# Performance work log

Hardware: AMD Instinct MI355X
Metric: run time of the kernel (lower is better)

The kernel has to match this reference:

```python
import jax, jax.numpy as jnp
import numpy as np

ALPHA = 0.1  # relu_alpha

def leaky(v, a=ALPHA):
    return jnp.where(v > 0, v, a * v)

def setup_inputs() -> dict:
    key = jax.random.key(0)
    ks = jax.random.split(key, 12)
    N, D, E, H = 50000, 128, 800000, 256
    x = jax.random.normal(ks[0], (N, D), dtype=jnp.float32)
    edge_index = jax.random.randint(ks[1], (2, E), 0, N, dtype=jnp.int64)
    def lin(k, i, o):
        s = 1.0 / np.sqrt(i)
        return jax.random.uniform(k, (i, o), jnp.float32, -s, s)
    return {
        "x": x,
        "edge_index": edge_index,
        "W_gcn": lin(ks[2], D, 512), "b_gcn": jnp.zeros((512,), jnp.float32),
        "W1": lin(ks[3], 512, H), "b1": jnp.zeros((H,), jnp.float32),
        "W2": lin(ks[4], H, H), "b2": jnp.zeros((H,), jnp.float32),
        "W3": lin(ks[5], H, H), "b3": jnp.zeros((H,), jnp.float32),
        "W_out": lin(ks[6], H, 1), "b_out": jnp.zeros((1,), jnp.float32),
    }

def gcn_conv(x, edge_index, W, b):
    N = x.shape[0]
    loop = jnp.arange(N, dtype=edge_index.dtype)
    src = jnp.concatenate([edge_index[0], loop])  # [E+N]
    dst = jnp.concatenate([edge_index[1], loop])
    h = x @ W  # [N, 512]
    deg = jax.ops.segment_sum(jnp.ones_like(dst, dtype=h.dtype), dst, num_segments=N)
    dinv = jnp.where(deg > 0, jax.lax.rsqrt(jnp.maximum(deg, 1e-12)), 0.0)
    norm = dinv[src] * dinv[dst]  # [E+N]
    msg = h[src] * norm[:, None]  # [E+N, 512] -- dominant memory traffic
    out = jax.ops.segment_sum(msg, dst, num_segments=N)
    return out + b

def reference(x, edge_index, W_gcn, b_gcn, W1, b1, W2, b2, W3, b3, W_out, b_out):
    h = gcn_conv(x, edge_index, W_gcn, b_gcn)
    h = leaky(h @ W1 + b1)
    h = leaky(h @ W2 + b2)
    h = leaky(h @ W3 + b3)
    return h @ W_out + b_out  # [N, 1]
```

## Files before the change

### kernel.cpp

```cpp
#include <hip/hip_runtime.h>
#include <hip/hip_bf16.h>
#include <cstdint>

#define ALPHA 0.1f
#define BCAP 3072

using bf16x8 = __attribute__((ext_vector_type(8))) short;
using f32x4  = __attribute__((ext_vector_type(4))) float;

__device__ __forceinline__ unsigned short f2bf(float f) {
    unsigned u = __builtin_bit_cast(unsigned, f);
    u += 0x7fff + ((u >> 16) & 1);
    return (unsigned short)(u >> 16);
}
__device__ __forceinline__ float bf2f(unsigned short h) {
    unsigned u = ((unsigned)h) << 16;
    return __builtin_bit_cast(float, u);
}
__device__ __forceinline__ float bflo(unsigned v) {
    return __builtin_bit_cast(float, v << 16);
}
__device__ __forceinline__ float bfhi(unsigned v) {
    return __builtin_bit_cast(float, v & 0xffff0000u);
}

__device__ __forceinline__ void async16(void* lds, const void* g) {
    __builtin_amdgcn_global_load_lds(
        reinterpret_cast<const unsigned int __attribute__((address_space(1)))*>(
            reinterpret_cast<uintptr_t>(g)),
        reinterpret_cast<unsigned int __attribute__((address_space(3)))*>(
            reinterpret_cast<uintptr_t>(lds)),
        16, 0, 0);
}


__global__ void zero_kernel(int* __restrict__ bcnt, float* __restrict__ outv, int nb, int n) {
    int i = blockIdx.x * blockDim.x + threadIdx.x;
    if (i < nb) bcnt[i] = 0;
    if (i < n) outv[i] = 0.f;
}


__global__ void passA_kernel(
    const int* __restrict__ ei, int* __restrict__ bcnt, unsigned* __restrict__ bkt,
    const float* __restrict__ Wg, const float* __restrict__ bg,
    const float* __restrict__ W1, const float* __restrict__ b1,
    const float* __restrict__ W2, const float* __restrict__ W3,
    unsigned short* __restrict__ WcT, float* __restrict__ bc,
    unsigned short* __restrict__ W2T, unsigned short* __restrict__ W3T,
    int E, int NB, int nA)
{
    __shared__ int lcnt[512];
    __shared__ int lbase[512];
    int blk = blockIdx.x, tid = threadIdx.x;

    if (blk < nA) {
        const int e0 = blk * 8192;
        for (int i = tid; i < NB; i += 256) lcnt[i] = 0;
        __syncthreads();
#pragma unroll 8
        for (int k = 0; k < 32; ++k) {
            int e = e0 + tid + k * 256;
            if (e < E) atomicAdd(&lcnt[ei[E + e] >> 7], 1);
        }
        __syncthreads();
        for (int i = tid; i < NB; i += 256) lbase[i] = atomicAdd(&bcnt[i], lcnt[i]);
        __syncthreads();
        for (int i = tid; i < NB; i += 256) lcnt[i] = 0;
        __syncthreads();
#pragma unroll 4
        for (int k = 0; k < 32; ++k) {
            int e = e0 + tid + k * 256;
            if (e < E) {
                int s = ei[e], d = ei[E + e];
                int b = d >> 7;
                int r = atomicAdd(&lcnt[b], 1);
                int pos = lbase[b] + r;
                if (pos < BCAP) bkt[(size_t)b * BCAP + pos] = ((unsigned)d << 16) | (unsigned)s;
            }
        }
    } else {
        int wb = blk - nA;
        if (wb < 128) {
            int m = wb, n = tid;
            float acc = 0.f;
#pragma unroll 8
            for (int k = 0; k < 512; ++k) acc += Wg[m * 512 + k] * W1[k * 256 + n];
            unsigned short h = f2bf(acc);
            WcT[n * 256 + m] = h;
            WcT[n * 256 + 128 + m] = f2bf(acc - bf2f(h));
        } else if (wb == 128) {
            int n = tid;
            float acc = b1[n];
#pragma unroll 8
            for (int k = 0; k < 512; ++k) acc += bg[k] * W1[k * 256 + n];
            bc[n] = acc;
        } else {
            int idx = (wb - 129) * 256 + tid;
            if (idx < 65536) {
                int n = idx >> 8, k = idx & 255;
                W2T[idx] = f2bf(W2[k * 256 + n]);
            } else {
                int i2 = idx - 65536;
                int n = i2 >> 8, k = i2 & 255;
                W3T[i2] = f2bf(W3[k * 256 + n]);
            }
        }
    }
}


__global__ void passB_kernel(
    const unsigned* __restrict__ bkt, const int* __restrict__ bcnt,
    const float4* __restrict__ x4,
    unsigned short* __restrict__ colT, int* __restrict__ cnt, uint2* __restrict__ xs,
    int N)
{
    __shared__ int lcnt[128];
    int b = blockIdx.x, tid = threadIdx.x;
    if (tid < 128) lcnt[tid] = 0;
    __syncthreads();
    int ne = bcnt[b]; if (ne > BCAP) ne = BCAP;
    for (int i = tid; i < ne; i += 256) {
        unsigned p = bkt[(size_t)b * BCAP + i];
        int d = p >> 16, s = p & 0xffff;
        int r = atomicAdd(&lcnt[d & 127], 1);
        if (r < 128) colT[((size_t)d << 7) | r] = (unsigned short)s;
    }
    __syncthreads();
    int n0 = b << 7;
    if (tid < 128 && n0 + tid < N) cnt[n0 + tid] = lcnt[tid];
    for (int i = tid; i < 4096; i += 256) {
        int node = n0 + (i >> 5);
        if (node >= N) break;
        float di = 1.0f / sqrtf((float)(lcnt[i >> 5] + 1));
        float4 v = x4[(size_t)node * 32 + (i & 31)];
        uint2 o;
        o.x = (unsigned)f2bf(di * v.x) | ((unsigned)f2bf(di * v.y) << 16);
        o.y = (unsigned)f2bf(di * v.z) | ((unsigned)f2bf(di * v.w) << 16);
        xs[(size_t)node * 32 + (i & 31)] = o;
    }
}


__global__ void agg_kernel(const unsigned* __restrict__ xs, const unsigned short* __restrict__ colT,
                           const int* __restrict__ cnt,
                           unsigned* __restrict__ aggp, int N) {
    int w = (blockIdx.x * blockDim.x + threadIdx.x) >> 6;
    int lane = threadIdx.x & 63;
    if (w >= N) return;
    int c = cnt[w];
    float di = 1.0f / sqrtf((float)(c + 1));
    unsigned vself = xs[(size_t)w * 64 + lane];
    float ax = bflo(vself), ay = bfhi(vself);
    const unsigned short* col = colT + ((size_t)w << 7);
    int e = c < 128 ? c : 128;
    int j = 0;
    for (; j + 8 <= e; j += 8) {
        unsigned short idx8[8];
        *reinterpret_cast<uint4*>(idx8) = *reinterpret_cast<const uint4*>(&col[j]);
        unsigned v0 = xs[(size_t)idx8[0] * 64 + lane];
        unsigned v1 = xs[(size_t)idx8[1] * 64 + lane];
        unsigned v2 = xs[(size_t)idx8[2] * 64 + lane];
        unsigned v3 = xs[(size_t)idx8[3] * 64 + lane];
        unsigned v4 = xs[(size_t)idx8[4] * 64 + lane];
        unsigned v5 = xs[(size_t)idx8[5] * 64 + lane];
        unsigned v6 = xs[(size_t)idx8[6] * 64 + lane];
        unsigned v7 = xs[(size_t)idx8[7] * 64 + lane];
        ax += bflo(v0) + bflo(v1) + bflo(v2) + bflo(v3)
            + bflo(v4) + bflo(v5) + bflo(v6) + bflo(v7);
        ay += bfhi(v0) + bfhi(v1) + bfhi(v2) + bfhi(v3)
            + bfhi(v4) + bfhi(v5) + bfhi(v6) + bfhi(v7);
    }
    for (; j + 4 <= e; j += 4) {
        unsigned short idx4[4];
        *reinterpret_cast<uint2*>(idx4) = *reinterpret_cast<const uint2*>(&col[j]);
        unsigned v0 = xs[(size_t)idx4[0] * 64 + lane];
        unsigned v1 = xs[(size_t)idx4[1] * 64 + lane];
        unsigned v2 = xs[(size_t)idx4[2] * 64 + lane];
        unsigned v3 = xs[(size_t)idx4[3] * 64 + lane];
        ax += bflo(v0) + bflo(v1) + bflo(v2) + bflo(v3);
        ay += bfhi(v0) + bfhi(v1) + bfhi(v2) + bfhi(v3);
    }
    for (; j < e; ++j) {
        unsigned v = xs[(size_t)col[j] * 64 + lane];
        ax += bflo(v);
        ay += bfhi(v);
    }
    float g0 = di * ax, g1 = di * ay;
    aggp[(size_t)w * 64 + lane] = (unsigned)f2bf(g0) | ((unsigned)f2bf(g1) << 16);
}


template <bool WRAP, bool HEAD>
__global__ __launch_bounds__(256) void gemm_k(
    const unsigned short* __restrict__ A, const unsigned short* __restrict__ Bt,
    const float* __restrict__ bias, unsigned short* __restrict__ C,
    const float* __restrict__ wo, const float* __restrict__ bo,
    float* __restrict__ outv, int M)
{
    constexpr int AK = WRAP ? 128 : 256;
    __shared__ unsigned short At[128 * 64];
    __shared__ unsigned short Bs[128 * 64];

    const int tid  = threadIdx.x;
    const int lane = tid & 63;
    const int wid  = tid >> 6;
    const int wrow = wid >> 1, wcol = wid & 1;
    const int l15 = lane & 15, l4 = lane >> 4;
    const int m0 = blockIdx.x * 128, n0 = blockIdx.y * 128;

    const int srow = lane >> 3;
    const int sq   = lane & 7;

    f32x4 acc[4][4] = {};

    for (int k0 = 0; k0 < 256; k0 += 64) {
        __syncthreads();
        const int ka = WRAP ? (k0 & 127) : k0;
#pragma unroll
        for (int i = 0; i < 4; ++i) {
            int c = wid + i * 4;
            int row = c * 8 + srow;
            int ks = (sq ^ (row & 7)) * 8;
            int gm = m0 + row; if (gm >= M) gm = M - 1;
            async16(&At[c * 512], &A[(size_t)gm * AK + ka + ks]);
            async16(&Bs[c * 512], &Bt[(size_t)(n0 + row) * 256 + k0 + ks]);
        }
        __syncthreads();

#pragma unroll
        for (int h = 0; h < 2; ++h) {
            bf16x8 af[4], bf[4];
#pragma unroll
            for (int mi = 0; mi < 4; ++mi) {
                int row = wrow * 64 + mi * 16 + l15;
                int ps = (h * 4 + l4) ^ (row & 7);
                af[mi] = *reinterpret_cast<const bf16x8*>(&At[row * 64 + ps * 8]);
            }
#pragma unroll
            for (int ni = 0; ni < 4; ++ni) {
                int row = wcol * 64 + ni * 16 + l15;
                int ps = (h * 4 + l4) ^ (row & 7);
                bf[ni] = *reinterpret_cast<const bf16x8*>(&Bs[row * 64 + ps * 8]);
            }
#pragma unroll
            for (int mi = 0; mi < 4; ++mi)
#pragma unroll
                for (int ni = 0; ni < 4; ++ni)
                    acc[mi][ni] = __builtin_amdgcn_mfma_f32_16x16x32_bf16(af[mi], bf[ni], acc[mi][ni], 0, 0, 0);
        }
    }

    if (!HEAD) {
#pragma unroll
        for (int mi = 0; mi < 4; ++mi) {
#pragma unroll
            for (int r = 0; r < 4; ++r) {
                int gm = m0 + wrow * 64 + mi * 16 + l4 * 4 + r;
                if (gm >= M) continue;
#pragma unroll
                for (int ni = 0; ni < 4; ++ni) {
                    int gn = n0 + wcol * 64 + ni * 16 + l15;
                    float v = acc[mi][ni][r] + bias[gn];
                    v = v > 0.f ? v : ALPHA * v;
                    C[(size_t)gm * 256 + gn] = f2bf(v);
                }
            }
        }
    } else {
        float bn[4], wn[4];
#pragma unroll
        for (int ni = 0; ni < 4; ++ni) {
            int gn = n0 + wcol * 64 + ni * 16 + l15;
            bn[ni] = bias[gn];
            wn[ni] = wo[gn];
        }
        float badd = (n0 == 0 && wcol == 0) ? bo[0] : 0.f;
#pragma unroll
        for (int mi = 0; mi < 4; ++mi) {
#pragma unroll
            for (int r = 0; r < 4; ++r) {
                float p = 0.f;
#pragma unroll
                for (int ni = 0; ni < 4; ++ni) {
                    float v = acc[mi][ni][r] + bn[ni];
                    v = v > 0.f ? v : ALPHA * v;
                    p += v * wn[ni];
                }
#pragma unroll
                for (int off = 1; off < 16; off <<= 1) p += __shfl_xor(p, off, 16);
                int gm = m0 + wrow * 64 + mi * 16 + l4 * 4 + r;
                if (l15 == 0 && gm < M) atomicAdd(&outv[gm], p + badd);
            }
        }
    }
}


extern "C" void kernel_launch(void* const* d_in, const int* in_sizes, int n_in,
                              void* d_out, int out_size, void* d_ws, size_t ws_size,
                              hipStream_t stream) {
    const float* x  = (const float*)d_in[0];
    const int*   ei = (const int*)d_in[1];
    const float* Wg = (const float*)d_in[2];
    const float* bg = (const float*)d_in[3];
    const float* W1 = (const float*)d_in[4];
    const float* b1 = (const float*)d_in[5];
    const float* W2 = (const float*)d_in[6];
    const float* b2 = (const float*)d_in[7];
    const float* W3 = (const float*)d_in[8];
    const float* b3 = (const float*)d_in[9];
    const float* Wo = (const float*)d_in[10];
    const float* bo = (const float*)d_in[11];
    float* out = (float*)d_out;

    const int N = in_sizes[0] / 128;
    const int E = in_sizes[1] / 2;
    const int NB = (N + 127) >> 7;

    char* ws = (char*)d_ws;
    unsigned* xs     = (unsigned*)ws; ws += (size_t)N * 64 * 4;
    unsigned* aggp   = (unsigned*)ws; ws += (size_t)N * 64 * 4;
    unsigned short* h1 = (unsigned short*)ws; ws += (size_t)N * 256 * 2;
    unsigned short* h2 = (unsigned short*)ws; ws += (size_t)N * 256 * 2;
    unsigned short* colT = (unsigned short*)ws; ws += (size_t)N * 128 * 2;
    unsigned* bkt = (unsigned*)ws; ws += (size_t)NB * BCAP * 4;
    int* bcnt  = (int*)ws;    ws += (size_t)(NB + 64) * 4;
    int* cnt   = (int*)ws;    ws += (size_t)N * 4;
    float* bc  = (float*)ws;  ws += 256 * 4;
    unsigned short* WcT = (unsigned short*)ws; ws += 256 * 256 * 2;
    unsigned short* W2T = (unsigned short*)ws; ws += 256 * 256 * 2;
    unsigned short* W3T = (unsigned short*)ws; ws += 256 * 256 * 2;

    zero_kernel<<<(N + 255) / 256, 256, 0, stream>>>(bcnt, out, NB, N);

    const int nA = (E + 8191) / 8192;
    passA_kernel<<<nA + 641, 256, 0, stream>>>(
        ei, bcnt, bkt, Wg, bg, W1, b1, W2, W3, WcT, bc, W2T, W3T, E, NB, nA);

    passB_kernel<<<NB, 256, 0, stream>>>(bkt, bcnt, (const float4*)x, colT, cnt, (uint2*)xs, N);

    agg_kernel<<<(N + 3) / 4, 256, 0, stream>>>(xs, colT, cnt, aggp, N);

    dim3 g((N + 127) / 128, 2);
    gemm_k<true,  false><<<g, 256, 0, stream>>>((const unsigned short*)aggp, WcT, bc, h1,
                                                nullptr, nullptr, nullptr, N);
    gemm_k<false, false><<<g, 256, 0, stream>>>(h1, W2T, b2, h2, nullptr, nullptr, nullptr, N);
    gemm_k<false, true ><<<g, 256, 0, stream>>>(h2, W3T, b3, nullptr, Wo, bo, out, N);
}
```

Before: 151.4 us.

## Stage bucket scatter and adjacency tile in LDS for coalesced global writes

```diff
diff --git a/kernel.cpp b/kernel.cpp
--- a/kernel.cpp
+++ b/kernel.cpp
@@ -50,18 +50,37 @@
     unsigned short* __restrict__ W2T, unsigned short* __restrict__ W3T,
     int E, int NB, int nA)
 {
+    __shared__ unsigned stage[8192];
     __shared__ int lcnt[512];
+    __shared__ int loff[512];
     __shared__ int lbase[512];
     int blk = blockIdx.x, tid = threadIdx.x;
 
     if (blk < nA) {
         const int e0 = blk * 8192;
+        const int tot = min(8192, E - e0);
         for (int i = tid; i < NB; i += 256) lcnt[i] = 0;
         __syncthreads();
 #pragma unroll 8
         for (int k = 0; k < 32; ++k) {
             int e = e0 + tid + k * 256;
             if (e < E) atomicAdd(&lcnt[ei[E + e] >> 7], 1);
+        }
+        __syncthreads();
+        if (tid < 64) {
+            int carry = 0;
+            for (int base = 0; base < NB; base += 64) {
+                int i = base + tid;
+                int v = (i < NB) ? lcnt[i] : 0;
+                int pre = v;
+#pragma unroll
+                for (int off = 1; off < 64; off <<= 1) {
+                    int t = __shfl_up(pre, off, 64);
+                    if (tid >= off) pre += t;
+                }
+                if (i < NB) loff[i] = carry + pre - v;
+                carry += __shfl(pre, 63, 64);
+            }
         }
         __syncthreads();
         for (int i = tid; i < NB; i += 256) lbase[i] = atomicAdd(&bcnt[i], lcnt[i]);
@@ -75,9 +94,15 @@
                 int s = ei[e], d = ei[E + e];
                 int b = d >> 7;
                 int r = atomicAdd(&lcnt[b], 1);
-                int pos = lbase[b] + r;
-                if (pos < BCAP) bkt[(size_t)b * BCAP + pos] = ((unsigned)d << 16) | (unsigned)s;
-            }
+                stage[loff[b] + r] = ((unsigned)d << 16) | (unsigned)s;
+            }
+        }
+        __syncthreads();
+        for (int i = tid; i < tot; i += 256) {
+            unsigned p = stage[i];
+            int b = p >> 23;
+            int pos = lbase[b] + (i - loff[b]);
+            if (pos < BCAP) bkt[(size_t)b * BCAP + pos] = p;
         }
     } else {
         int wb = blk - nA;
@@ -116,6 +141,7 @@
     unsigned short* __restrict__ colT, int* __restrict__ cnt, uint2* __restrict__ xs,
     int N)
 {
+    __shared__ unsigned short img[128 * 128];
     __shared__ int lcnt[128];
     int b = blockIdx.x, tid = threadIdx.x;
     if (tid < 128) lcnt[tid] = 0;
@@ -125,14 +151,17 @@
         unsigned p = bkt[(size_t)b * BCAP + i];
         int d = p >> 16, s = p & 0xffff;
         int r = atomicAdd(&lcnt[d & 127], 1);
-        if (r < 128) colT[((size_t)d << 7) | r] = (unsigned short)s;
+        if (r < 128) img[((d & 127) << 7) | r] = (unsigned short)s;
     }
     __syncthreads();
     int n0 = b << 7;
-    if (tid < 128 && n0 + tid < N) cnt[n0 + tid] = lcnt[tid];
-    for (int i = tid; i < 4096; i += 256) {
+    int nrows = min(128, N - n0);
+    if (tid < 128 && tid < nrows) cnt[n0 + tid] = lcnt[tid];
+    uint2* dst = reinterpret_cast<uint2*>(colT + (size_t)n0 * 128);
+    const uint2* srcp = reinterpret_cast<const uint2*>(img);
+    for (int i = tid; i < nrows * 32; i += 256) dst[i] = srcp[i];
+    for (int i = tid; i < nrows * 32; i += 256) {
         int node = n0 + (i >> 5);
-        if (node >= N) break;
         float di = 1.0f / sqrtf((float)(lcnt[i >> 5] + 1));
         float4 v = x4[(size_t)node * 32 + (i & 31)];
         uint2 o;
@@ -324,7 +353,7 @@
     unsigned* aggp   = (unsigned*)ws; ws += (size_t)N * 64 * 4;
     unsigned short* h1 = (unsigned short*)ws; ws += (size_t)N * 256 * 2;
     unsigned short* h2 = (unsigned short*)ws; ws += (size_t)N * 256 * 2;
-    unsigned short* colT = (unsigned short*)ws; ws += (size_t)N * 128 * 2;
+    unsigned short* colT = (unsigned short*)ws; ws += (size_t)(NB * 128) * 128 * 2;
     unsigned* bkt = (unsigned*)ws; ws += (size_t)NB * BCAP * 4;
     int* bcnt  = (int*)ws;    ws += (size_t)(NB + 64) * 4;
     int* cnt   = (int*)ws;    ws += (size_t)N * 4;
```

Measured after the change: 146.0 us. 3.5% less time.
